# Kernel optimization log

Measured on AMD Instinct MI355X. Metric: run time of the kernel, lower is better.

The kernel has to match this reference:

```python
import jax, jax.numpy as jnp
import numpy as np

V, E, C, H = 32000, 512, 512, 1024  # vocab, embed_dim, context_dim, hidden_dim
NB, NL = 3, 2                       # layer_structure = [2, 2, 2]
EPS = 1e-5


def _ln(x, g, b):
    m = jnp.mean(x, axis=-1, keepdims=True)
    v = jnp.mean(jnp.square(x - m), axis=-1, keepdims=True)
    return (x - m) * jax.lax.rsqrt(v + EPS) * g + b


def setup_inputs() -> dict:
    key = jax.random.key(0)
    ks = jax.random.split(key, 8)
    B, S = 4, 1024
    std = 0.02
    return {
        "input_ids": jax.random.randint(ks[0], (B, S), 0, V),
        "embed_table": std * jax.random.normal(ks[1], (V, E), jnp.float32),
        "en_g": jnp.ones((E,), jnp.float32),
        "en_b": jnp.zeros((E,), jnp.float32),
        # all FNN linears are H x H since context_dim + embed_dim == hidden_dim
        "Wb": std * jax.random.normal(ks[2], (NB, NL, H, H), jnp.float32),
        "bb": jnp.zeros((NB, NL, H), jnp.float32),
        "cn_g": jnp.ones((NB, C), jnp.float32),
        "cn_b": jnp.zeros((NB, C), jnp.float32),
        "tn_g": jnp.ones((NB, E), jnp.float32),
        "tn_b": jnp.zeros((NB, E), jnp.float32),
        "out_W": std * jax.random.normal(ks[3], (V, C), jnp.float32),
        "out_b": jnp.zeros((V,), jnp.float32),
    }


def reference(input_ids, embed_table, en_g, en_b, Wb, bb,
              cn_g, cn_b, tn_g, tn_b, out_W, out_b):
    # Embedding + LayerNorm: [B, S, E]
    x = _ln(embed_table[input_ids], en_g, en_b)
    # In the original, context is reset to zeros at every timestep t, so the
    # per-t Python loop is an embarrassingly parallel map over (B, S):
    ctx = jnp.zeros(x.shape[:-1] + (C,), x.dtype)
    tok = x
    for bi in range(NB):
        h = jnp.concatenate([ctx, tok], axis=-1)  # [B, S, H]
        for li in range(NL):
            h = jax.nn.relu(jnp.einsum('bsh,oh->bso', h, Wb[bi, li]) + bb[bi, li])
        ctx = _ln(ctx + h[..., :C], cn_g[bi], cn_b[bi])
        tok = _ln(tok + h[..., C:], tn_g[bi], tn_b[bi])
    # token_output applied to updated token vector (requires E == C)
    logits = jnp.einsum('bse,ve->bsv', tok, out_W) + out_b
    return logits
```

## Files before the change

### kernel.cpp

```cpp
#include <hip/hip_runtime.h>

typedef __bf16 bf16x8 __attribute__((ext_vector_type(8)));
typedef __bf16 bf16x4 __attribute__((ext_vector_type(4)));
typedef __bf16 bf16x2 __attribute__((ext_vector_type(2)));
typedef float  f32x4  __attribute__((ext_vector_type(4)));

#define T_TOK 4096
#define EDIM 512
#define HDIM 1024
#define VOCAB 32000

__device__ __forceinline__ void async_copy16(const void* g, void* l) {
    __builtin_amdgcn_global_load_lds(
        (const __attribute__((address_space(1))) unsigned int*)g,
        (__attribute__((address_space(3))) unsigned int*)l, 16, 0, 0);
}

__global__ void cvt_f32_bf16(const float4* __restrict__ src, bf16x4* __restrict__ dst, int n4) {
    int i = blockIdx.x * blockDim.x + threadIdx.x;
    if (i < n4) {
        float4 v = src[i];
        bf16x4 o = { (__bf16)v.x, (__bf16)v.y, (__bf16)v.z, (__bf16)v.w };
        dst[i] = o;
    }
}

__device__ __forceinline__ void breduce2(float& s1, float& s2, float* sh) {
    #pragma unroll
    for (int off = 32; off >= 1; off >>= 1) {
        s1 += __shfl_xor(s1, off);
        s2 += __shfl_xor(s2, off);
    }
    int wid = threadIdx.x >> 6;
    __syncthreads();
    if ((threadIdx.x & 63) == 0) { sh[wid] = s1; sh[4 + wid] = s2; }
    __syncthreads();
    s1 = sh[0] + sh[1] + sh[2] + sh[3];
    s2 = sh[4] + sh[5] + sh[6] + sh[7];
}

__global__ void embed_ln(const int* __restrict__ ids, const float* __restrict__ tab,
                         const float* __restrict__ g, const float* __restrict__ b,
                         float* __restrict__ tok, float* __restrict__ ctx,
                         __bf16* __restrict__ h) {
    __shared__ float sh[8];
    const int t = blockIdx.x, tid = threadIdx.x;
    const float2* row = (const float2*)(tab + (size_t)ids[t] * EDIM);
    float2 v = row[tid];
    float s1 = v.x + v.y;
    float s2 = v.x * v.x + v.y * v.y;
    breduce2(s1, s2, sh);
    const float mean = s1 * (1.0f / EDIM);
    const float var  = s2 * (1.0f / EDIM) - mean * mean;
    const float rstd = rsqrtf(var + 1e-5f);
    float2 gg = ((const float2*)g)[tid];
    float2 bb = ((const float2*)b)[tid];
    float y0 = (v.x - mean) * rstd * gg.x + bb.x;
    float y1 = (v.y - mean) * rstd * gg.y + bb.y;
    ((float2*)(tok + (size_t)t * EDIM))[tid] = make_float2(y0, y1);
    ((float2*)(ctx + (size_t)t * EDIM))[tid] = make_float2(0.f, 0.f);
    __bf16* hrow = h + (size_t)t * HDIM;
    ((bf16x2*)hrow)[tid]         = bf16x2{ (__bf16)0.f, (__bf16)0.f };
    ((bf16x2*)(hrow + EDIM))[tid] = bf16x2{ (__bf16)y0, (__bf16)y1 };
}

__global__ void resid_ln(const float* __restrict__ h32, float* __restrict__ ctx,
                         float* __restrict__ tok,
                         const float* __restrict__ cg, const float* __restrict__ cb,
                         const float* __restrict__ tg, const float* __restrict__ tb,
                         __bf16* __restrict__ hn) {
    __shared__ float sh[8];
    const int t = blockIdx.x, tid = threadIdx.x;
    const float2* hrow = (const float2*)(h32 + (size_t)t * HDIM);
    __bf16* hnrow = hn + (size_t)t * HDIM;

    {
        float2 c  = ((float2*)(ctx + (size_t)t * EDIM))[tid];
        float2 hv = hrow[tid];
        float x0 = c.x + hv.x, x1 = c.y + hv.y;
        float s1 = x0 + x1, s2 = x0 * x0 + x1 * x1;
        breduce2(s1, s2, sh);
        const float mean = s1 * (1.0f / EDIM);
        const float rstd = rsqrtf(s2 * (1.0f / EDIM) - mean * mean + 1e-5f);
        float2 gg = ((const float2*)cg)[tid];
        float2 bb = ((const float2*)cb)[tid];
        float y0 = (x0 - mean) * rstd * gg.x + bb.x;
        float y1 = (x1 - mean) * rstd * gg.y + bb.y;
        ((float2*)(ctx + (size_t)t * EDIM))[tid] = make_float2(y0, y1);
        ((bf16x2*)hnrow)[tid] = bf16x2{ (__bf16)y0, (__bf16)y1 };
    }
    {
        float2 tv = ((float2*)(tok + (size_t)t * EDIM))[tid];
        float2 hv = hrow[256 + tid];
        float x0 = tv.x + hv.x, x1 = tv.y + hv.y;
        float s1 = x0 + x1, s2 = x0 * x0 + x1 * x1;
        breduce2(s1, s2, sh);
        const float mean = s1 * (1.0f / EDIM);
        const float rstd = rsqrtf(s2 * (1.0f / EDIM) - mean * mean + 1e-5f);
        float2 gg = ((const float2*)tg)[tid];
        float2 bb = ((const float2*)tb)[tid];
        float y0 = (x0 - mean) * rstd * gg.x + bb.x;
        float y1 = (x1 - mean) * rstd * gg.y + bb.y;
        ((float2*)(tok + (size_t)t * EDIM))[tid] = make_float2(y0, y1);
        ((bf16x2*)(hnrow + EDIM))[tid] = bf16x2{ (__bf16)y0, (__bf16)y1 };
    }
}

__global__ __launch_bounds__(256, 2)
void gemm_bt(const __bf16* __restrict__ A, int lda,
             const __bf16* __restrict__ B, int ldb,
             const float* __restrict__ bias,
             __bf16* __restrict__ Cb, float* __restrict__ Cf,
             int ldc, int K, int do_relu) {
    __shared__ __align__(16) __bf16 sA[128 * 32];
    __shared__ __align__(16) __bf16 sB[128 * 32];
    const int tid = threadIdx.x;
    const int m0 = blockIdx.x * 128, n0 = blockIdx.y * 128;
    const int wid = tid >> 6, lane = tid & 63;
    const int wm = (wid >> 1) * 64, wn = (wid & 1) * 64;
    const int lr = lane & 15, lq = lane >> 4;

    f32x4 acc[4][4] = {};

    const __bf16* Abase = A + (size_t)m0 * lda;
    const __bf16* Bbase = B + (size_t)n0 * ldb;
    const int r0 = tid >> 2;
    const int q0 = tid & 3;

    for (int k0 = 0; k0 < K; k0 += 32) {
        const __bf16* Ak = Abase + k0 + q0 * 8;
        const __bf16* Bk = Bbase + k0 + q0 * 8;
        async_copy16(Ak + (size_t)r0 * lda,        sA + (size_t)tid * 8);
        async_copy16(Ak + (size_t)(r0 + 64) * lda, sA + (size_t)(tid + 256) * 8);
        async_copy16(Bk + (size_t)r0 * ldb,        sB + (size_t)tid * 8);
        async_copy16(Bk + (size_t)(r0 + 64) * ldb, sB + (size_t)(tid + 256) * 8);
        __syncthreads();

        bf16x8 af[4], bfr[4];
        #pragma unroll
        for (int mi = 0; mi < 4; mi++)
            af[mi] = *(const bf16x8*)(sA + (wm + mi * 16 + lr) * 32 + lq * 8);
        #pragma unroll
        for (int ni = 0; ni < 4; ni++)
            bfr[ni] = *(const bf16x8*)(sB + (wn + ni * 16 + lr) * 32 + lq * 8);
        #pragma unroll
        for (int mi = 0; mi < 4; mi++)
            #pragma unroll
            for (int ni = 0; ni < 4; ni++)
                acc[mi][ni] = __builtin_amdgcn_mfma_f32_16x16x32_bf16(
                    af[mi], bfr[ni], acc[mi][ni], 0, 0, 0);
        __syncthreads();
    }

    #pragma unroll
    for (int mi = 0; mi < 4; mi++) {
        const int rbase = m0 + wm + mi * 16 + lq * 4;
        #pragma unroll
        for (int ni = 0; ni < 4; ni++) {
            const int col = n0 + wn + ni * 16 + lr;
            const float bv = bias[col];
            #pragma unroll
            for (int r = 0; r < 4; r++) {
                float v = acc[mi][ni][r] + bv;
                if (do_relu) v = fmaxf(v, 0.f);
                const size_t idx = (size_t)(rbase + r) * ldc + col;
                if (Cf) Cf[idx] = v;
                if (Cb) Cb[idx] = (__bf16)v;
            }
        }
    }
}

extern "C" void kernel_launch(void* const* d_in, const int* in_sizes, int n_in,
                              void* d_out, int out_size, void* d_ws, size_t ws_size,
                              hipStream_t stream) {
    const int*   ids  = (const int*)d_in[0];
    const float* tab  = (const float*)d_in[1];
    const float* en_g = (const float*)d_in[2];
    const float* en_b = (const float*)d_in[3];
    const float* Wb   = (const float*)d_in[4];
    const float* bb   = (const float*)d_in[5];
    const float* cn_g = (const float*)d_in[6];
    const float* cn_b = (const float*)d_in[7];
    const float* tn_g = (const float*)d_in[8];
    const float* tn_b = (const float*)d_in[9];
    const float* outW = (const float*)d_in[10];
    const float* outb = (const float*)d_in[11];
    float* out = (float*)d_out;

    char* ws = (char*)d_ws;
    float*  tok  = (float*)ws;  ws += (size_t)T_TOK * EDIM * 4;
    float*  ctx  = (float*)ws;  ws += (size_t)T_TOK * EDIM * 4;
    float*  h32  = (float*)ws;  ws += (size_t)T_TOK * HDIM * 4;
    __bf16* hA   = (__bf16*)ws; ws += (size_t)T_TOK * HDIM * 2;
    __bf16* hB   = (__bf16*)ws; ws += (size_t)T_TOK * HDIM * 2;
    __bf16* Wb16 = (__bf16*)ws; ws += (size_t)6 * HDIM * HDIM * 2;
    __bf16* oW16 = (__bf16*)ws; ws += (size_t)VOCAB * EDIM * 2;

    const int nW  = 6 * HDIM * HDIM;
    const int nOW = VOCAB * EDIM;
    cvt_f32_bf16<<<(nW / 4 + 255) / 256, 256, 0, stream>>>((const float4*)Wb, (bf16x4*)Wb16, nW / 4);
    cvt_f32_bf16<<<(nOW / 4 + 255) / 256, 256, 0, stream>>>((const float4*)outW, (bf16x4*)oW16, nOW / 4);

    embed_ln<<<T_TOK, 256, 0, stream>>>(ids, tab, en_g, en_b, tok, ctx, hA);

    for (int bi = 0; bi < 3; bi++) {
        gemm_bt<<<dim3(32, 8), 256, 0, stream>>>(
            hA, HDIM, Wb16 + (size_t)(bi * 2 + 0) * HDIM * HDIM, HDIM,
            bb + (size_t)(bi * 2 + 0) * HDIM, hB, nullptr, HDIM, HDIM, 1);
        gemm_bt<<<dim3(32, 8), 256, 0, stream>>>(
            hB, HDIM, Wb16 + (size_t)(bi * 2 + 1) * HDIM * HDIM, HDIM,
            bb + (size_t)(bi * 2 + 1) * HDIM, nullptr, h32, HDIM, HDIM, 1);
        resid_ln<<<T_TOK, 256, 0, stream>>>(
            h32, ctx, tok, cn_g + bi * EDIM, cn_b + bi * EDIM,
            tn_g + bi * EDIM, tn_b + bi * EDIM, hA);
    }

    gemm_bt<<<dim3(32, VOCAB / 128), 256, 0, stream>>>(
        hA + EDIM, HDIM, oW16, EDIM, outb, nullptr, out, VOCAB, EDIM, 0);
}
```

Before: 976.9 us.

## Add dedicated 256x256 pipelined logits GEMM and skip zero-context half in first block

Adds a specialised 512-thread logits GEMM kernel with 256x256 tiles, swizzled LDS staging via async global-to-LDS copies, double-buffered K loop interleaved with MFMA, and a grouped workgroup order for L2 reuse. It also shrinks the first FNN layer's K dimension to 512, because the context half of the input is all zeros at block 0. The aim is to cut the dominant vocab-projection cost and avoid redundant math. The trade-offs are higher register and LDS pressure, and hand-tuned waitcnt logic that may be fragile.

```diff
diff --git a/kernel.cpp b/kernel.cpp
--- a/kernel.cpp
+++ b/kernel.cpp
@@ -171,6 +171,124 @@
     }
 }
 
+#define NKT 8
+
+__device__ __forceinline__ void stage_half(const __bf16* __restrict__ gsrc, int ld,
+                                           __bf16* __restrict__ lds_half, int tid) {
+    #pragma unroll
+    for (int c = 0; c < 2; c++) {
+        const int g   = tid + c * 512;
+        const int row = g >> 3;
+        const int lc  = (g & 7) ^ (row & 7);
+        async_copy16(gsrc + (size_t)row * ld + lc * 8, lds_half + (size_t)g * 8);
+    }
+}
+
+__global__ __launch_bounds__(512, 2)
+void gemm_logits(const __bf16* __restrict__ A, const __bf16* __restrict__ B,
+                 const float* __restrict__ bias, float* __restrict__ C) {
+    __shared__ __align__(16) __bf16 sA[4 * 128 * 64];
+    __shared__ __align__(16) __bf16 sB[4 * 128 * 64];
+    const int tid = threadIdx.x;
+
+    const int wg  = blockIdx.x;
+    const int swz = (wg & 7) * 250 + (wg >> 3);
+    const int cc  = swz % 250;
+    const int mt  = (swz / 250) * 2 + (cc & 1);
+    const int nt  = cc >> 1;
+    const int m0 = mt << 8, n0 = nt << 8;
+
+    const int wid = tid >> 6, lane = tid & 63;
+    const int wm  = (wid >> 2) << 7;
+    const int wn  = (wid & 3) << 6;
+    const int lr  = lane & 15, lq = lane >> 4;
+    const int ah  = wm >> 7;
+    const int bh  = wn >> 7;
+    const int br0 = wn & 64;
+
+    f32x4 acc[8][4] = {};
+
+    const __bf16* Abase = A + (size_t)m0 * HDIM;
+    const __bf16* Bbase = B + (size_t)n0 * EDIM;
+
+    stage_half(Abase,                           HDIM, sA,            tid);
+    stage_half(Abase + (size_t)128 * HDIM,      HDIM, sA + 8192,     tid);
+    stage_half(Bbase,                           EDIM, sB,            tid);
+    stage_half(Bbase + (size_t)128 * EDIM,      EDIM, sB + 8192,     tid);
+    stage_half(Bbase + 64,                      EDIM, sB + 2 * 8192, tid);
+    stage_half(Bbase + (size_t)128 * EDIM + 64, EDIM, sB + 3 * 8192, tid);
+    asm volatile("s_waitcnt vmcnt(4)" ::: "memory");
+    __builtin_amdgcn_s_barrier();
+
+    #pragma unroll 1
+    for (int u = 0; u < NKT; u++) {
+        const int par = u & 1, nxt = par ^ 1;
+        const __bf16* sAh = sA + (par * 2 + ah) * 8192;
+        const __bf16* sBh = sB + (par * 2 + bh) * 8192;
+        bf16x8 bfr[4][2];
+        #pragma unroll
+        for (int q = 0; q < 4; q++) {
+            if (q == 0) {
+                #pragma unroll
+                for (int ni = 0; ni < 4; ni++)
+                    #pragma unroll
+                    for (int ks = 0; ks < 2; ks++) {
+                        const int row = br0 + ni * 16 + lr;
+                        bfr[ni][ks] = *(const bf16x8*)(sBh + (row << 6) +
+                                        (((ks * 4 + lq) ^ (row & 7)) << 3));
+                    }
+            }
+            bf16x8 af[2][2];
+            #pragma unroll
+            for (int mi = 0; mi < 2; mi++)
+                #pragma unroll
+                for (int ks = 0; ks < 2; ks++) {
+                    const int row = (q * 2 + mi) * 16 + lr;
+                    af[mi][ks] = *(const bf16x8*)(sAh + (row << 6) +
+                                    (((ks * 4 + lq) ^ (row & 7)) << 3));
+                }
+            if (q == 0 && u + 1 < NKT)
+                stage_half(Abase + (u + 1) * 64,                      HDIM, sA + (nxt * 2) * 8192,     tid);
+            if (q == 1 && u + 1 < NKT)
+                stage_half(Abase + (size_t)128 * HDIM + (u + 1) * 64, HDIM, sA + (nxt * 2 + 1) * 8192, tid);
+            if (q == 2 && u + 2 < NKT)
+                stage_half(Bbase + (u + 2) * 64,                      EDIM, sB + (par * 2) * 8192,     tid);
+            if (q == 3 && u + 2 < NKT)
+                stage_half(Bbase + (size_t)128 * EDIM + (u + 2) * 64, EDIM, sB + (par * 2 + 1) * 8192, tid);
+            __builtin_amdgcn_s_barrier();
+            asm volatile("s_waitcnt lgkmcnt(0)" ::: "memory");
+            __builtin_amdgcn_s_setprio(1);
+            #pragma unroll
+            for (int mi = 0; mi < 2; mi++)
+                #pragma unroll
+                for (int ni = 0; ni < 4; ni++)
+                    #pragma unroll
+                    for (int ks = 0; ks < 2; ks++)
+                        acc[q * 2 + mi][ni] = __builtin_amdgcn_mfma_f32_16x16x32_bf16(
+                            af[mi][ks], bfr[ni][ks], acc[q * 2 + mi][ni], 0, 0, 0);
+            __builtin_amdgcn_s_setprio(0);
+            if (q == 3) {
+                if (u < NKT - 2)       { asm volatile("s_waitcnt vmcnt(4)" ::: "memory"); }
+                else if (u == NKT - 2) { asm volatile("s_waitcnt vmcnt(0)" ::: "memory"); }
+            }
+            __builtin_amdgcn_s_barrier();
+        }
+    }
+
+    #pragma unroll
+    for (int mi = 0; mi < 8; mi++) {
+        const int row = m0 + wm + mi * 16 + lq * 4;
+        #pragma unroll
+        for (int ni = 0; ni < 4; ni++) {
+            const int col = n0 + wn + ni * 16 + lr;
+            const float bv = bias[col];
+            #pragma unroll
+            for (int r = 0; r < 4; r++)
+                C[(size_t)(row + r) * VOCAB + col] = acc[mi][ni][r] + bv;
+        }
+    }
+}
+
 extern "C" void kernel_launch(void* const* d_in, const int* in_sizes, int n_in,
                               void* d_out, int out_size, void* d_ws, size_t ws_size,
                               hipStream_t stream) {
@@ -205,9 +323,15 @@
     embed_ln<<<T_TOK, 256, 0, stream>>>(ids, tab, en_g, en_b, tok, ctx, hA);
 
     for (int bi = 0; bi < 3; bi++) {
-        gemm_bt<<<dim3(32, 8), 256, 0, stream>>>(
-            hA, HDIM, Wb16 + (size_t)(bi * 2 + 0) * HDIM * HDIM, HDIM,
-            bb + (size_t)(bi * 2 + 0) * HDIM, hB, nullptr, HDIM, HDIM, 1);
+        if (bi == 0) {
+            gemm_bt<<<dim3(32, 8), 256, 0, stream>>>(
+                hA + EDIM, HDIM, Wb16 + 512, HDIM,
+                bb, hB, nullptr, HDIM, 512, 1);
+        } else {
+            gemm_bt<<<dim3(32, 8), 256, 0, stream>>>(
+                hA, HDIM, Wb16 + (size_t)(bi * 2 + 0) * HDIM * HDIM, HDIM,
+                bb + (size_t)(bi * 2 + 0) * HDIM, hB, nullptr, HDIM, HDIM, 1);
+        }
         gemm_bt<<<dim3(32, 8), 256, 0, stream>>>(
             hB, HDIM, Wb16 + (size_t)(bi * 2 + 1) * HDIM * HDIM, HDIM,
             bb + (size_t)(bi * 2 + 1) * HDIM, nullptr, h32, HDIM, HDIM, 1);
@@ -216,6 +340,5 @@
             tn_g + bi * EDIM, tn_b + bi * EDIM, hA);
     }
 
-    gemm_bt<<<dim3(32, VOCAB / 128), 256, 0, stream>>>(
-        hA + EDIM, HDIM, oW16, EDIM, outb, nullptr, out, VOCAB, EDIM, 0);
-}
+    gemm_logits<<<2000, 512, 0, stream>>>(hA + EDIM, oW16, outb, out);
+}
```

Measured after the change: 966.8 us. About the same (-1.0%).
